# Optimization experiments

Measured on AMD Instinct MI355X. Metric: run time of the kernel, lower is better.

## Reference

```python
import jax, jax.numpy as jnp
import numpy as np

SEQ, B = 512, 2048
H, OUT = 512, 1
IN = 32  # linearIn input_size; x feature dim = IN - OUT = 31


def setup_inputs() -> dict:
    key = jax.random.key(0)
    ks = jax.random.split(key, 12)
    u = lambda k, shape, lim: jax.random.uniform(k, shape, jnp.float32, -lim, lim)
    lim_in = 1.0 / np.sqrt(IN)
    lim_h = 1.0 / np.sqrt(H)
    return {
        "x": jax.random.normal(ks[0], (SEQ, B, IN - OUT), jnp.float32),
        # initial states (torch eval path uses randn*0.1)
        "h0": jax.random.normal(ks[1], (B, H), jnp.float32) * 0.1,
        "c0": jax.random.normal(ks[2], (B, H), jnp.float32) * 0.1,
        "y0": jax.random.normal(ks[3], (B, OUT), jnp.float32) * 0.1,
        # linearIn
        "W_in": u(ks[4], (H, IN), lim_in),
        "b_in": u(ks[5], (H,), lim_in),
        # single-layer LSTM (gate order i, f, g, o as in PyTorch)
        "W_ih": u(ks[6], (4 * H, H), lim_h),
        "W_hh": u(ks[7], (4 * H, H), lim_h),
        "b_ih": u(ks[8], (4 * H,), lim_h),
        "b_hh": u(ks[9], (4 * H,), lim_h),
        # linearOut
        "W_out": u(ks[10], (OUT, H), lim_h),
        "b_out": u(ks[11], (OUT,), lim_h),
    }


def reference(x, h0, c0, y0, W_in, b_in, W_ih, W_hh, b_ih, b_hh, W_out, b_out):
    b_gate = b_ih + b_hh

    def step(carry, xt):
        h, c, y = carry  # [B,H], [B,H], [B,OUT]
        inp = jnp.concatenate([xt, y], axis=-1)          # [B, IN]
        x0 = jax.nn.relu(inp @ W_in.T + b_in)            # [B, H]
        gates = x0 @ W_ih.T + h @ W_hh.T + b_gate        # [B, 4H]
        i, f, g, o = jnp.split(gates, 4, axis=-1)
        c = jax.nn.sigmoid(f) * c + jax.nn.sigmoid(i) * jnp.tanh(g)
        h = jax.nn.sigmoid(o) * jnp.tanh(c)
        y = h @ W_out.T + b_out                          # [B, OUT]
        return (h, c, y), y

    _, ys = jax.lax.scan(step, (h0, c0, y0), x)
    return ys  # [SEQ, B, OUT]
```

## Files before the change

### kernel.cpp

```cpp
#include <hip/hip_runtime.h>
#include <hip/hip_bf16.h>
#include <stdint.h>

#define SEQ   512
#define BATCH 2048
#define HID   512
#define XF    31

typedef __bf16 bf16_t;
typedef bf16_t bf16x8 __attribute__((ext_vector_type(8)));
typedef bf16_t bf16x4 __attribute__((ext_vector_type(4)));
typedef float  f32x4  __attribute__((ext_vector_type(4)));

__device__ __forceinline__ void gload16(const void* g, void* lds) {
    __builtin_amdgcn_global_load_lds(
        (const __attribute__((address_space(1))) void*)g,
        (__attribute__((address_space(3))) void*)lds,
        16, 0, 0);
}

__device__ __forceinline__ float sigmoid_f(float x) {
    return 1.f / (1.f + __expf(-x));
}
__device__ __forceinline__ float tanh_f(float x) {
    float e = __expf(2.f * x);
    return 1.f - 2.f / (e + 1.f);
}

__global__ void prep_w(const float* __restrict__ W_ih, const float* __restrict__ W_hh,
                       bf16_t* __restrict__ Wcat) {
    const int j = blockIdx.x;
    for (int k = threadIdx.x; k < 1024; k += 256) {
        float v = (k < 512) ? W_ih[(size_t)j * 512 + k]
                            : W_hh[(size_t)j * 512 + (k - 512)];
        Wcat[(size_t)j * 1024 + k] = (bf16_t)v;
    }
}

__global__ void prep_state(const float* __restrict__ h0, const float* __restrict__ c0,
                           bf16_t* __restrict__ H0, float* __restrict__ Cbuf,
                           float* __restrict__ out_all) {
    const int b = blockIdx.x;
    for (int d = threadIdx.x; d < 512; d += 256) {
        H0[(size_t)b * 512 + d]   = (bf16_t)h0[(size_t)b * 512 + d];
        Cbuf[(size_t)b * 512 + d] = c0[(size_t)b * 512 + d];
        out_all[(size_t)b * 512 + d] = 0.f;
    }
}

__global__ void prep_bias(const float* __restrict__ b_ih, const float* __restrict__ b_hh,
                          float* __restrict__ bg) {
    int j = blockIdx.x * 256 + threadIdx.x;
    bg[j] = b_ih[j] + b_hh[j];
}

__global__ void prep_wb(const float* __restrict__ W_in,
                        bf16_t* __restrict__ Wbh, bf16_t* __restrict__ Wbl) {
    int idx = blockIdx.x * 256 + threadIdx.x;
    float v = W_in[idx];
    bf16_t h = (bf16_t)v;
    Wbh[idx] = h;
    Wbl[idx] = (bf16_t)(v - (float)h);
}

__global__ __launch_bounds__(512, 1) void step_fused(
    const float*  __restrict__ x_t,
    const float*  __restrict__ yprev,
    const bf16_t* __restrict__ Wbh,
    const bf16_t* __restrict__ Wbl,
    const float*  __restrict__ b_in,
    const bf16_t* __restrict__ Hin,
    bf16_t*       __restrict__ Hout,
    float*        __restrict__ Cbuf,
    const bf16_t* __restrict__ Wcat,
    const float*  __restrict__ b_gate,
    const float*  __restrict__ W_out,
    const float*  __restrict__ b_out,
    float*        __restrict__ yout)
{
    __shared__ __align__(16) char smem[163840];
    float (*Gs0)[128] = (float (*)[128])smem;
    float (*Gs1)[128] = (float (*)[128])(smem + 65536);

    const int tid  = threadIdx.x;
    const int lane = tid & 63;
    const int wid  = tid >> 6;
    const int wm   = wid >> 2;
    const int wn   = (wid >> 1) & 1;
    const int wk   = wid & 1;

    const int bid  = blockIdx.x;
    const int xcd  = bid & 7;
    const int slot = bid >> 3;
    const int mb   = (xcd >> 1) * 4 + (slot & 3);
    const int nb   = (xcd & 1) * 8 + (slot >> 2);

    const int r  = lane & 15, q = lane >> 4;
    const int lr  = lane >> 3;
    const int lcs = ((lane & 7) ^ lr) * 8;
    const int kob = (((wk << 2) + q) ^ (r & 7)) * 16;

    bf16x8 xh[8], xl[8];
#pragma unroll
    for (int g = 0; g < 8; ++g) {
        const int row = mb * 128 + g * 16 + r;
        const float* bp = x_t + (size_t)row * XF + q * 8;
        float tmp[8];
#pragma unroll
        for (int j = 0; j < 7; ++j) tmp[j] = bp[j];
        const float* p7 = (q == 3) ? (yprev + row) : (bp + 7);
        tmp[7] = *p7;
#pragma unroll
        for (int j = 0; j < 8; ++j) {
            bf16_t h = (bf16_t)tmp[j];
            xh[g][j] = h;
            xl[g][j] = (bf16_t)(tmp[j] - (float)h);
        }
    }

    f32x4 acc[4][4];
#pragma unroll
    for (int mi = 0; mi < 4; ++mi)
#pragma unroll
        for (int ni = 0; ni < 4; ++ni) {
            f32x4 z = {0.f, 0.f, 0.f, 0.f};
            acc[mi][ni] = z;
        }

    auto stageAB = [&](int dst, int kt) {
        const int k0 = (kt - 8) * 64;
#pragma unroll
        for (int iss = 0; iss < 2; ++iss) {
            const int r0 = wid * 16 + iss * 8;
            gload16(Hin + (size_t)(mb * 128 + r0 + lr) * 512 + k0 + lcs,
                    smem + (size_t)dst * 16384 + r0 * 128);
        }
#pragma unroll
        for (int iss = 0; iss < 2; ++iss) {
            const int r0   = wid * 16 + iss * 8;
            const int nloc = r0 + lr;
            const int j    = (nloc >> 5) * 512 + nb * 32 + (nloc & 31);
            gload16(Wcat + (size_t)j * 1024 + kt * 64 + lcs,
                    smem + 65536 + (size_t)dst * 16384 + r0 * 128);
        }
    };
    auto stageB2 = [&](int dst, int kt) {
#pragma unroll
        for (int iss = 0; iss < 2; ++iss) {
            const int r0   = wid * 16 + iss * 8;
            const int nloc = r0 + lr;
            const int j    = (nloc >> 5) * 512 + nb * 32 + (nloc & 31);
            gload16(Wcat + (size_t)j * 1024 + kt * 64 + lcs,
                    smem + 131072 + (size_t)dst * 16384 + r0 * 128);
        }
    };

    stageAB(0, 8);
    stageAB(1, 9);
#pragma unroll
    for (int kt = 8; kt < 16; ++kt) {
        if (kt + 2 < 16) stageAB((kt + 2) & 3, kt + 2);
        if (kt < 14) {
            asm volatile("s_waitcnt vmcnt(8)" ::: "memory");
        } else if (kt == 14) {
            asm volatile("s_waitcnt vmcnt(4)" ::: "memory");
        } else {
            asm volatile("s_waitcnt vmcnt(0)" ::: "memory");
        }
        __builtin_amdgcn_s_barrier();
        __builtin_amdgcn_sched_barrier(0);

        const int cur = kt & 3;
        const char* Ab = smem + (size_t)cur * 16384;
        const char* Bb = smem + 65536 + (size_t)cur * 16384;
        bf16x8 af[4], bfr[4];
#pragma unroll
        for (int mi = 0; mi < 4; ++mi)
            af[mi] = *(const bf16x8*)(Ab + (wm * 64 + mi * 16 + r) * 128 + kob);
#pragma unroll
        for (int ni = 0; ni < 4; ++ni)
            bfr[ni] = *(const bf16x8*)(Bb + (wn * 64 + ni * 16 + r) * 128 + kob);
#pragma unroll
        for (int mi = 0; mi < 4; ++mi)
#pragma unroll
            for (int ni = 0; ni < 4; ++ni)
                acc[mi][ni] = __builtin_amdgcn_mfma_f32_16x16x32_bf16(
                    af[mi], bfr[ni], acc[mi][ni], 0, 0, 0);
    }

    __syncthreads();

    bf16x8 wfh[4], wfl[4];
    float4 bi4[4];
#pragma unroll
    for (int u = 0; u < 4; ++u) {
        const int dt = wid * 4 + u;
        const size_t wo_ = (size_t)(dt * 16 + r) * 32 + q * 8;
        wfh[u] = *(const bf16x8*)&Wbh[wo_];
        wfl[u] = *(const bf16x8*)&Wbl[wo_];
        bi4[u] = *(const float4*)&b_in[dt * 16 + q * 4];
    }
    stageB2(0, 0);
    stageB2(1, 1);

#pragma unroll
    for (int u = 0; u < 4; ++u) {
        const int dt = wid * 4 + u;
#pragma unroll
        for (int g = 0; g < 8; ++g) {
            f32x4 pa = {0.f, 0.f, 0.f, 0.f};
            pa = __builtin_amdgcn_mfma_f32_16x16x32_bf16(wfh[u], xh[g], pa, 0, 0, 0);
            pa = __builtin_amdgcn_mfma_f32_16x16x32_bf16(wfh[u], xl[g], pa, 0, 0, 0);
            pa = __builtin_amdgcn_mfma_f32_16x16x32_bf16(wfl[u], xh[g], pa, 0, 0, 0);
            bf16x4 hv;
            hv[0] = (bf16_t)fmaxf(pa[0] + bi4[u].x, 0.f);
            hv[1] = (bf16_t)fmaxf(pa[1] + bi4[u].y, 0.f);
            hv[2] = (bf16_t)fmaxf(pa[2] + bi4[u].z, 0.f);
            hv[3] = (bf16_t)fmaxf(pa[3] + bi4[u].w, 0.f);
            const int c  = dt * 2 + (q >> 1);
            const int cs = (c & ~7) | ((c & 7) ^ (r & 7));
            *(bf16x4*)(smem + (size_t)(g * 16 + r) * 1024 + cs * 16 + (q & 1) * 8) = hv;
        }
    }

    __syncthreads();

#pragma unroll
    for (int kt = 0; kt < 8; ++kt) {
        if (kt < 7) {
            asm volatile("s_waitcnt vmcnt(2)" ::: "memory");
        } else {
            asm volatile("s_waitcnt vmcnt(0)" ::: "memory");
        }
        __builtin_amdgcn_s_barrier();
        __builtin_amdgcn_sched_barrier(0);

        const char* Bb = smem + 131072 + (size_t)(kt & 1) * 16384;
        bf16x8 af[4], bfr[4];
#pragma unroll
        for (int mi = 0; mi < 4; ++mi)
            af[mi] = *(const bf16x8*)(smem + (size_t)(wm * 64 + mi * 16 + r) * 1024
                                      + kt * 128 + kob);
#pragma unroll
        for (int ni = 0; ni < 4; ++ni)
            bfr[ni] = *(const bf16x8*)(Bb + (wn * 64 + ni * 16 + r) * 128 + kob);
#pragma unroll
        for (int mi = 0; mi < 4; ++mi)
#pragma unroll
            for (int ni = 0; ni < 4; ++ni)
                acc[mi][ni] = __builtin_amdgcn_mfma_f32_16x16x32_bf16(
                    af[mi], bfr[ni], acc[mi][ni], 0, 0, 0);
        __builtin_amdgcn_s_barrier();
        if (kt + 2 < 8) stageB2(kt & 1, kt + 2);
    }

    const int row    = tid >> 2;
    const int dq     = (tid & 3) * 8;
    const int b_glob = mb * 128 + row;

    float cv[8], wo[8];
    *(float4*)&cv[0] = *(const float4*)&Cbuf[(size_t)b_glob * 512 + nb * 32 + dq];
    *(float4*)&cv[4] = *(const float4*)&Cbuf[(size_t)b_glob * 512 + nb * 32 + dq + 4];
    *(float4*)&wo[0] = *(const float4*)&W_out[nb * 32 + dq];
    *(float4*)&wo[4] = *(const float4*)&W_out[nb * 32 + dq + 4];
    const float bo = b_out[0];

    __syncthreads();

    {
        float (*G)[128] = wk ? Gs1 : Gs0;
#pragma unroll
        for (int mi = 0; mi < 4; ++mi)
#pragma unroll
            for (int ni = 0; ni < 4; ++ni)
#pragma unroll
                for (int rr = 0; rr < 4; ++rr) {
                    const int gr = wm * 64 + mi * 16 + q * 4 + rr;
                    const int gc = wn * 64 + ni * 16 + r;
                    G[gr][gc ^ ((gr & 7) << 2)] = acc[mi][ni][rr];
                }
    }
    __syncthreads();

    {
        const int sx = (row & 7) << 2;
        float gv[4][8];
#pragma unroll
        for (int u = 0; u < 2; ++u) {
            const int cb = (dq + 4 * u) ^ sx;
#pragma unroll
            for (int g = 0; g < 4; ++g) {
                f32x4 a0 = *(const f32x4*)&Gs0[row][g * 32 + cb];
                f32x4 a1 = *(const f32x4*)&Gs1[row][g * 32 + cb];
#pragma unroll
                for (int j = 0; j < 4; ++j) gv[g][u * 4 + j] = a0[j] + a1[j];
            }
        }
        float bgv[4][8];
#pragma unroll
        for (int g = 0; g < 4; ++g) {
            *(float4*)&bgv[g][0] = *(const float4*)&b_gate[g * 512 + nb * 32 + dq];
            *(float4*)&bgv[g][4] = *(const float4*)&b_gate[g * 512 + nb * 32 + dq + 4];
        }
        float cnew[8];
        bf16_t hv[8];
        float yp = 0.f;
#pragma unroll
        for (int ii = 0; ii < 8; ++ii) {
            float is = sigmoid_f(gv[0][ii] + bgv[0][ii]);
            float fs = sigmoid_f(gv[1][ii] + bgv[1][ii]);
            float gt = tanh_f(gv[2][ii] + bgv[2][ii]);
            float os = sigmoid_f(gv[3][ii] + bgv[3][ii]);
            float c_new = fs * cv[ii] + is * gt;
            float hval  = os * tanh_f(c_new);
            cnew[ii] = c_new;
            hv[ii]   = (bf16_t)hval;
            yp += hval * wo[ii];
        }
        const size_t base = (size_t)b_glob * 512 + nb * 32 + dq;
        *(float4*)&Cbuf[base]     = *(const float4*)&cnew[0];
        *(float4*)&Cbuf[base + 4] = *(const float4*)&cnew[4];
        *(bf16x8*)&Hout[base]     = *(const bf16x8*)&hv[0];

        yp += __shfl_xor(yp, 1);
        yp += __shfl_xor(yp, 2);
        if ((tid & 3) == 0)
            atomicAdd(&yout[b_glob], yp + ((nb == 0) ? bo : 0.f));
    }
}

extern "C" void kernel_launch(void* const* d_in, const int* in_sizes, int n_in,
                              void* d_out, int out_size, void* d_ws, size_t ws_size,
                              hipStream_t stream) {
    const float* x     = (const float*)d_in[0];
    const float* h0    = (const float*)d_in[1];
    const float* c0    = (const float*)d_in[2];
    const float* y0    = (const float*)d_in[3];
    const float* W_in  = (const float*)d_in[4];
    const float* b_in  = (const float*)d_in[5];
    const float* W_ih  = (const float*)d_in[6];
    const float* W_hh  = (const float*)d_in[7];
    const float* b_ih  = (const float*)d_in[8];
    const float* b_hh  = (const float*)d_in[9];
    const float* W_out = (const float*)d_in[10];
    const float* b_out = (const float*)d_in[11];
    float* out = (float*)d_out;

    char* ws = (char*)d_ws;
    bf16_t* Wcat  = (bf16_t*)(ws);
    bf16_t* Hb0   = (bf16_t*)(ws + (4u << 20));
    bf16_t* Hb1   = (bf16_t*)(ws + (6u << 20));
    float*  Cbuf  = (float*)(ws + (8u << 20));
    float*  bgate = (float*)(ws + (12u << 20));
    bf16_t* Wbh   = (bf16_t*)(ws + (12u << 20) + (16u << 10));
    bf16_t* Wbl   = (bf16_t*)(ws + (12u << 20) + (64u << 10));
    bf16_t* Hb[2] = { Hb0, Hb1 };

    prep_w    <<<2048, 256, 0, stream>>>(W_ih, W_hh, Wcat);
    prep_state<<<2048, 256, 0, stream>>>(h0, c0, Hb[0], Cbuf, out);
    prep_bias <<<8,    256, 0, stream>>>(b_ih, b_hh, bgate);
    prep_wb   <<<64,   256, 0, stream>>>(W_in, Wbh, Wbl);

    for (int t = 0; t < SEQ; ++t) {
        const float* yprev = (t == 0) ? y0 : (out + (size_t)(t - 1) * BATCH);
        step_fused<<<256, 512, 0, stream>>>(
            x + (size_t)t * BATCH * XF, yprev, Wbh, Wbl, b_in,
            Hb[t & 1], Hb[(t + 1) & 1], Cbuf, Wcat, bgate, W_out, b_out,
            out + (size_t)t * BATCH);
    }
    (void)in_sizes; (void)n_in; (void)out_size; (void)ws_size;
}
```

Before: 10.19 ms.

## Process two K tiles per barrier, vectorize x loads, hoist gate bias loads

The K loop over the B operand now handles both double-buffer halves between barriers, so four barrier/wait rounds replace eight and two stages are issued per round. The cost is a full vmcnt(0) wait each round, which reduces overlap between staging and compute. The per-row x loads become two unaligned float4 loads, with y preloaded up front. The b_gate loads are moved ahead of the syncthreads so their latency overlaps with it.

```diff
diff --git a/kernel.cpp b/kernel.cpp
--- a/kernel.cpp
+++ b/kernel.cpp
@@ -17,6 +17,12 @@
         (const __attribute__((address_space(1))) void*)g,
         (__attribute__((address_space(3))) void*)lds,
         16, 0, 0);
+}
+
+__device__ __forceinline__ float4 ld4u(const float* p) {
+    float4 v;
+    __builtin_memcpy(&v, p, 16);
+    return v;
 }
 
 __device__ __forceinline__ float sigmoid_f(float x) {
@@ -100,16 +106,25 @@
     const int lcs = ((lane & 7) ^ lr) * 8;
     const int kob = (((wk << 2) + q) ^ (r & 7)) * 16;
 
+    float yv[8];
+    if (q == 3) {
+#pragma unroll
+        for (int g = 0; g < 8; ++g) yv[g] = yprev[mb * 128 + g * 16 + r];
+    }
+    const bool q3 = (q == 3);
     bf16x8 xh[8], xl[8];
 #pragma unroll
     for (int g = 0; g < 8; ++g) {
         const int row = mb * 128 + g * 16 + r;
         const float* bp = x_t + (size_t)row * XF + q * 8;
+        float4 f0 = ld4u(bp);
+        float4 f1 = ld4u(bp + (q3 ? 3 : 4));
         float tmp[8];
-#pragma unroll
-        for (int j = 0; j < 7; ++j) tmp[j] = bp[j];
-        const float* p7 = (q == 3) ? (yprev + row) : (bp + 7);
-        tmp[7] = *p7;
+        tmp[0] = f0.x; tmp[1] = f0.y; tmp[2] = f0.z; tmp[3] = f0.w;
+        tmp[4] = q3 ? f1.y : f1.x;
+        tmp[5] = q3 ? f1.z : f1.y;
+        tmp[6] = q3 ? f1.w : f1.z;
+        tmp[7] = q3 ? yv[g] : f1.w;
 #pragma unroll
         for (int j = 0; j < 8; ++j) {
             bf16_t h = (bf16_t)tmp[j];
@@ -226,32 +241,34 @@
     __syncthreads();
 
 #pragma unroll
-    for (int kt = 0; kt < 8; ++kt) {
-        if (kt < 7) {
-            asm volatile("s_waitcnt vmcnt(2)" ::: "memory");
-        } else {
-            asm volatile("s_waitcnt vmcnt(0)" ::: "memory");
-        }
+    for (int si = 0; si < 4; ++si) {
+        asm volatile("s_waitcnt vmcnt(0)" ::: "memory");
         __builtin_amdgcn_s_barrier();
         __builtin_amdgcn_sched_barrier(0);
-
-        const char* Bb = smem + 131072 + (size_t)(kt & 1) * 16384;
-        bf16x8 af[4], bfr[4];
-#pragma unroll
-        for (int mi = 0; mi < 4; ++mi)
-            af[mi] = *(const bf16x8*)(smem + (size_t)(wm * 64 + mi * 16 + r) * 1024
-                                      + kt * 128 + kob);
-#pragma unroll
-        for (int ni = 0; ni < 4; ++ni)
-            bfr[ni] = *(const bf16x8*)(Bb + (wn * 64 + ni * 16 + r) * 128 + kob);
-#pragma unroll
-        for (int mi = 0; mi < 4; ++mi)
+#pragma unroll
+        for (int half = 0; half < 2; ++half) {
+            const int kt = si * 2 + half;
+            const char* Bb = smem + 131072 + (size_t)half * 16384;
+            bf16x8 af[4], bfr[4];
+#pragma unroll
+            for (int mi = 0; mi < 4; ++mi)
+                af[mi] = *(const bf16x8*)(smem + (size_t)(wm * 64 + mi * 16 + r) * 1024
+                                          + kt * 128 + kob);
 #pragma unroll
             for (int ni = 0; ni < 4; ++ni)
-                acc[mi][ni] = __builtin_amdgcn_mfma_f32_16x16x32_bf16(
-                    af[mi], bfr[ni], acc[mi][ni], 0, 0, 0);
+                bfr[ni] = *(const bf16x8*)(Bb + (wn * 64 + ni * 16 + r) * 128 + kob);
+#pragma unroll
+            for (int mi = 0; mi < 4; ++mi)
+#pragma unroll
+                for (int ni = 0; ni < 4; ++ni)
+                    acc[mi][ni] = __builtin_amdgcn_mfma_f32_16x16x32_bf16(
+                        af[mi], bfr[ni], acc[mi][ni], 0, 0, 0);
+        }
         __builtin_amdgcn_s_barrier();
-        if (kt + 2 < 8) stageB2(kt & 1, kt + 2);
+        if (si < 3) {
+            stageB2(0, si * 2 + 2);
+            stageB2(1, si * 2 + 3);
+        }
     }
 
     const int row    = tid >> 2;
@@ -263,6 +280,12 @@
     *(float4*)&cv[4] = *(const float4*)&Cbuf[(size_t)b_glob * 512 + nb * 32 + dq + 4];
     *(float4*)&wo[0] = *(const float4*)&W_out[nb * 32 + dq];
     *(float4*)&wo[4] = *(const float4*)&W_out[nb * 32 + dq + 4];
+    float bgv[4][8];
+#pragma unroll
+    for (int g = 0; g < 4; ++g) {
+        *(float4*)&bgv[g][0] = *(const float4*)&b_gate[g * 512 + nb * 32 + dq];
+        *(float4*)&bgv[g][4] = *(const float4*)&b_gate[g * 512 + nb * 32 + dq + 4];
+    }
     const float bo = b_out[0];
 
     __syncthreads();
@@ -295,12 +318,6 @@
 #pragma unroll
                 for (int j = 0; j < 4; ++j) gv[g][u * 4 + j] = a0[j] + a1[j];
             }
-        }
-        float bgv[4][8];
-#pragma unroll
-        for (int g = 0; g < 4; ++g) {
-            *(float4*)&bgv[g][0] = *(const float4*)&b_gate[g * 512 + nb * 32 + dq];
-            *(float4*)&bgv[g][4] = *(const float4*)&b_gate[g * 512 + nb * 32 + dq + 4];
         }
         float cnew[8];
         bf16_t hv[8];
```

Result: slower. 11.11 ms (+9.0%).
